# Kernel tuning notes

Hardware: AMD Instinct MI355X
Metric: run time of the kernel (lower is better)

## Reference

```python
import jax, jax.numpy as jnp
import numpy as np

FEA_DIM = 256
NUM_HEADS = 8
B, N = 32, 48


def setup_inputs() -> dict:
    key = jax.random.key(0)
    ks = jax.random.split(key, 30)
    d = FEA_DIM
    inp = {
        "async_fea": jax.random.normal(ks[0], (B, N, d), dtype=jnp.float32),
        "sync_fea": jax.random.normal(ks[1], (B, N, d), dtype=jnp.float32),
        "async_adj": jax.random.randint(ks[2], (B, N, N), 0, 2, dtype=jnp.int32),
        "sync_adj": jax.random.randint(ks[3], (B, N, N), 0, 2, dtype=jnp.int32),
    }
    i = 4
    for pref in ("a_", "s_"):
        for nm in ("Wq", "Wk", "Wv", "Wo", "Wm"):
            inp[pref + nm] = 0.02 * jax.random.normal(ks[i], (d, d), dtype=jnp.float32); i += 1
            inp[pref + nm.replace("W", "b")] = 0.02 * jax.random.normal(ks[i], (d,), dtype=jnp.float32); i += 1
    return inp


def _aggregate(x_src, adj, fallback, Wq, bq, Wk, bk, Wv, bv, Wo, bo, Wm, bm):
    """For each target t: self-attention among neighbor set {s : adj[b,s,t] > 0}
    of x_src, mean-pool over neighbors, divide by count again, linear map.
    Targets with no neighbors fall back to `fallback`."""
    Bb, Nn, D = x_src.shape
    H = NUM_HEADS
    dh = D // H
    q = (x_src @ Wq.T + bq).reshape(Bb, Nn, H, dh)
    k = (x_src @ Wk.T + bk).reshape(Bb, Nn, H, dh)
    v = (x_src @ Wv.T + bv).reshape(Bb, Nn, H, dh)
    # shared pairwise scores among source nodes: [B, H, Q, K]
    scores = jnp.einsum("bqhd,bkhd->bhqk", q, k) / jnp.sqrt(jnp.float32(dh))
    # neighbor mask per target: adj[b, s, t] > 0 -> m[b, t, s]
    m = jnp.transpose(adj > 0, (0, 2, 1))  # [B, T, S] bool
    # per-target masked softmax over keys: logits [B, T, H, Q, K]
    key_bias = jnp.where(m[:, :, None, None, :], 0.0, -1e9)
    attn = jax.nn.softmax(scores[:, None] + key_bias, axis=-1)  # [B,T,H,Q,K]
    out = jnp.einsum("bthqk,bkhd->bthqd", attn, v).reshape(Bb, Nn, Nn, D)  # [B,T,Q,D]
    out = out @ Wo.T + bo
    mf = m.astype(out.dtype)  # [B, T, Q]
    cnt = mf.sum(-1)  # [B, T]
    denom = jnp.maximum(cnt, 1.0)
    # torch: mean over valid queries, then / edge_cnt  => sum / cnt^2
    pooled = jnp.einsum("btq,btqd->btd", mf, out) / (denom * denom)[..., None]
    mapped = pooled @ Wm.T + bm
    return jnp.where((cnt > 0)[..., None], mapped, fallback)


def reference(async_fea, sync_fea, async_adj, sync_adj,
              a_Wq, a_bq, a_Wk, a_bk, a_Wv, a_bv, a_Wo, a_bo, a_Wm, a_bm,
              s_Wq, s_bq, s_Wk, s_bk, s_Wv, s_bv, s_Wo, s_bo, s_Wm, s_bm):
    refined_async = _aggregate(sync_fea, sync_adj, async_fea,
                               a_Wq, a_bq, a_Wk, a_bk, a_Wv, a_bv, a_Wo, a_bo, a_Wm, a_bm)
    refined_sync = _aggregate(async_fea, async_adj, sync_fea,
                              s_Wq, s_bq, s_Wk, s_bk, s_Wv, s_bv, s_Wo, s_bo, s_Wm, s_bm)
    return jnp.concatenate([refined_async, refined_sync, async_fea, sync_fea], axis=2)
```

## Files before the change

### kernel.cpp

```cpp
#include <hip/hip_runtime.h>

#define DD 256
#define HH 8
#define NN 48
#define BB 32

typedef __attribute__((ext_vector_type(8))) short short8v;
typedef __attribute__((ext_vector_type(4))) float f32x4;

__device__ __forceinline__ unsigned short f2bf(float f) {
    union { float f; unsigned u; } v; v.f = f;
    unsigned u = v.u;
    return (unsigned short)((u + 0x7FFFu + ((u >> 16) & 1u)) >> 16);
}

__device__ __forceinline__ short8v cvt8(const float* p) {
    float4 lo = *(const float4*)p;
    float4 hi = *(const float4*)(p + 4);
    union { uint4 u; short8v s; } r;
    asm("v_cvt_pk_bf16_f32 %0, %1, %2" : "=v"(r.u.x) : "v"(lo.x), "v"(lo.y));
    asm("v_cvt_pk_bf16_f32 %0, %1, %2" : "=v"(r.u.y) : "v"(lo.z), "v"(lo.w));
    asm("v_cvt_pk_bf16_f32 %0, %1, %2" : "=v"(r.u.z) : "v"(hi.x), "v"(hi.y));
    asm("v_cvt_pk_bf16_f32 %0, %1, %2" : "=v"(r.u.w) : "v"(hi.z), "v"(hi.w));
    return r.s;
}

__global__ __launch_bounds__(256) void qkv_fold(
    const float* __restrict__ async_fea, const float* __restrict__ sync_fea,
    const float* __restrict__ aWq, const float* __restrict__ abq,
    const float* __restrict__ aWk, const float* __restrict__ abk,
    const float* __restrict__ aWv, const float* __restrict__ abv,
    const float* __restrict__ aWm, const float* __restrict__ aWo, const float* __restrict__ abo,
    const float* __restrict__ sWq, const float* __restrict__ sbq,
    const float* __restrict__ sWk, const float* __restrict__ sbk,
    const float* __restrict__ sWv, const float* __restrict__ sbv,
    const float* __restrict__ sWm, const float* __restrict__ sWo, const float* __restrict__ sbo,
    float* __restrict__ QKV0, float* __restrict__ QKV1,
    unsigned short* __restrict__ Wcb0, unsigned short* __restrict__ Wcb1,
    float* __restrict__ bc0, float* __restrict__ bc1)
{
    __shared__ float smem[2304];
    int bid = blockIdx.x, tid = threadIdx.x;
    int wave = tid >> 6, lane = tid & 63;
    int l15 = lane & 15, l16 = (lane >> 4) << 3;

    if (bid < 576) {
        int agg = bid / 288, rem = bid % 288;
        int rt = rem / 12, ct = rem % 12;
        int row0 = rt * 64 + wave * 16;
        int col0 = ct * 64;
        int mat = ct >> 2;
        const float* X = agg ? async_fea : sync_fea;
        const float* W;
        const float* bias;
        if (agg == 0) {
            W    = (mat == 0) ? aWq : (mat == 1) ? aWk : aWv;
            bias = (mat == 0) ? abq : (mat == 1) ? abk : abv;
        } else {
            W    = (mat == 0) ? sWq : (mat == 1) ? sWk : sWv;
            bias = (mat == 0) ? sbq : (mat == 1) ? sbk : sbv;
        }
        const float* Xp = X + (row0 + l15) * 256 + l16;
        const float* Wp = W + ((ct & 3) * 64 + l15) * 256 + l16;
        f32x4 acc[4] = {{0,0,0,0},{0,0,0,0},{0,0,0,0},{0,0,0,0}};
        #pragma unroll
        for (int kk = 0; kk < 256; kk += 32) {
            short8v a = cvt8(Xp + kk);
            #pragma unroll
            for (int j = 0; j < 4; ++j) {
                short8v b = cvt8(Wp + j * 16 * 256 + kk);
                acc[j] = __builtin_amdgcn_mfma_f32_16x16x32_bf16(a, b, acc[j], 0, 0, 0);
            }
        }
        float* outQ = agg ? QKV1 : QKV0;
        #pragma unroll
        for (int j = 0; j < 4; ++j) {
            float bv = bias[(ct & 3) * 64 + j * 16 + l15];
            #pragma unroll
            for (int i = 0; i < 4; ++i) {
                int m = ((lane >> 4) << 2) + i;
                outQ[(row0 + m) * 768 + col0 + j * 16 + l15] = acc[j][i] + bv;
            }
        }
    } else {
        int fid = bid - 576;
        int agg = fid >> 4, tile = fid & 15;
        int cb = (tile >> 2) * 64, db = (tile & 3) * 64;
        const float* Wm = agg ? sWm : aWm;
        const float* Wo = agg ? sWo : aWo;
        const float* bo = agg ? sbo : abo;
        unsigned short* Wcb = agg ? Wcb1 : Wcb0;
        float* bc = agg ? bc1 : bc0;
        int crow = cb + wave * 16 + l15;
        const float* Wmp = Wm + crow * 256 + l16;
        f32x4 acc[4] = {{0,0,0,0},{0,0,0,0},{0,0,0,0},{0,0,0,0}};
        for (int ch = 0; ch < 8; ++ch) {
            __syncthreads();
            #pragma unroll
            for (int l = 0; l < 8; ++l) {
                int e = l * 256 + tid;
                int ii = e >> 6, dd = e & 63;
                smem[dd * 36 + ii] = Wo[(ch * 32 + ii) * 256 + db + dd];
            }
            __syncthreads();
            short8v a = cvt8(Wmp + ch * 32);
            #pragma unroll
            for (int j = 0; j < 4; ++j) {
                float* sp = &smem[(j * 16 + l15) * 36 + l16];
                float4 lo = *(const float4*)sp;
                float4 hi = *(const float4*)(sp + 4);
                union { uint4 u; short8v s; } rb;
                asm("v_cvt_pk_bf16_f32 %0, %1, %2" : "=v"(rb.u.x) : "v"(lo.x), "v"(lo.y));
                asm("v_cvt_pk_bf16_f32 %0, %1, %2" : "=v"(rb.u.y) : "v"(lo.z), "v"(lo.w));
                asm("v_cvt_pk_bf16_f32 %0, %1, %2" : "=v"(rb.u.z) : "v"(hi.x), "v"(hi.y));
                asm("v_cvt_pk_bf16_f32 %0, %1, %2" : "=v"(rb.u.w) : "v"(hi.z), "v"(hi.w));
                acc[j] = __builtin_amdgcn_mfma_f32_16x16x32_bf16(a, rb.s, acc[j], 0, 0, 0);
            }
        }
        #pragma unroll
        for (int j = 0; j < 4; ++j)
            #pragma unroll
            for (int i = 0; i < 4; ++i) {
                int c = cb + wave * 16 + ((lane >> 4) << 2) + i;
                int d = db + j * 16 + l15;
                Wcb[c * 256 + d] = f2bf(acc[j][i]);
            }
        if ((tile & 3) == 0) {
            int r = tid >> 2, s = tid & 3;
            const float* wmr = Wm + (cb + r) * 256 + s * 64;
            const float* bor = bo + s * 64;
            float a = 0.f;
            #pragma unroll
            for (int i = 0; i < 64; ++i) a += wmr[i] * bor[i];
            a += __shfl_xor(a, 1);
            a += __shfl_xor(a, 2);
            if (s == 0) bc[cb + r] = a;
        }
    }
}

__global__ __launch_bounds__(384) void mega_kernel(
    const float* __restrict__ QKV0, const float* __restrict__ QKV1,
    const int* __restrict__ sync_adj, const int* __restrict__ async_adj,
    const unsigned short* __restrict__ Wcb0, const unsigned short* __restrict__ Wcb1,
    const float* __restrict__ bc0, const float* __restrict__ bc1,
    const float* __restrict__ abm, const float* __restrict__ sbm,
    const float* __restrict__ async_fea, const float* __restrict__ sync_fea,
    float* __restrict__ out)
{
    __shared__ float E_lds[8 * 48 * 49];
    __shared__ float msk[12 * 48];
    __shared__ float invd[12][384];
    __shared__ float yv[12][384];
    __shared__ unsigned short P_lds[16 * 264];
    __shared__ float cnt_l[12];

    int bid = blockIdx.x, tid = threadIdx.x;
    int agg = bid >> 7, rem = bid & 127;
    int b = rem >> 2, tg = rem & 3;
    int wave = tid >> 6, lane = tid & 63;
    int l15 = lane & 15, g = lane >> 4, l16 = g << 3;

    const float* QKV = agg ? QKV1 : QKV0;
    const int*   adj = agg ? async_adj : sync_adj;
    const float* fb  = agg ? sync_fea : async_fea;
    int row_base = b * 48 + tg * 12;

    {
        const float4* fb4 = (const float4*)fb;
        float4* out4 = (float4*)out;
        #pragma unroll
        for (int l = 0; l < 2; ++l) {
            int e = l * 384 + tid;
            int r = e >> 6, c = e & 63;
            out4[(row_base + r) * 256 + 128 + agg * 64 + c] =
                fb4[(row_base + r) * 64 + c];
        }
    }

    for (int e = tid; e < 576; e += 384) {
        int tt = e / 48, s = e % 48;
        msk[tt * 48 + s] = (adj[(b * 48 + s) * 48 + tg * 12 + tt] > 0) ? 1.f : 0.f;
    }

    const float scale = 0.17677669529663687f;
    #pragma unroll
    for (int jj = 0; jj < 4; ++jj) {
        int job = wave * 4 + jj;
        int h = job / 3, qt = job % 3;
        short8v a = cvt8(QKV + (b * 48 + qt * 16 + l15) * 768 + h * 32 + l16);
        f32x4 acc[3];
        #pragma unroll
        for (int kt = 0; kt < 3; ++kt) {
            short8v kb = cvt8(QKV + (b * 48 + kt * 16 + l15) * 768 + 256 + h * 32 + l16);
            f32x4 z = {0.f, 0.f, 0.f, 0.f};
            acc[kt] = __builtin_amdgcn_mfma_f32_16x16x32_bf16(a, kb, z, 0, 0, 0);
        }
        float sc[3][4], rm[4];
        #pragma unroll
        for (int i = 0; i < 4; ++i) {
            #pragma unroll
            for (int kt = 0; kt < 3; ++kt) sc[kt][i] = acc[kt][i] * scale;
            rm[i] = fmaxf(fmaxf(sc[0][i], sc[1][i]), sc[2][i]);
        }
        #pragma unroll
        for (int m = 1; m <= 8; m <<= 1) {
            #pragma unroll
            for (int i = 0; i < 4; ++i) rm[i] = fmaxf(rm[i], __shfl_xor(rm[i], m));
        }
        #pragma unroll
        for (int kt = 0; kt < 3; ++kt)
            #pragma unroll
            for (int i = 0; i < 4; ++i)
                E_lds[(h * 48 + qt * 16 + g * 4 + i) * 49 + kt * 16 + l15] =
                    __expf(sc[kt][i] - rm[i]);
    }
    __syncthreads();

    if (tid < 12) {
        float c = 0.f;
        for (int s = 0; s < 48; ++s) c += msk[tid * 48 + s];
        cnt_l[tid] = c;
    }

    {
        float erow[48];
        #pragma unroll
        for (int kk = 0; kk < 48; ++kk) erow[kk] = E_lds[tid * 49 + kk];
        int q = tid % 48;
        #pragma unroll
        for (int tt = 0; tt < 12; ++tt) {
            const float4* m4p = (const float4*)&msk[tt * 48];
            float s = 0.f;
            #pragma unroll
            for (int k4 = 0; k4 < 12; ++k4) {
                float4 m4 = m4p[k4];
                s += m4.x * erow[4 * k4] + m4.y * erow[4 * k4 + 1]
                   + m4.z * erow[4 * k4 + 2] + m4.w * erow[4 * k4 + 3];
            }
            float mq = msk[tt * 48 + q];
            invd[tt][tid] = (mq > 0.f) ? (1.f / s) : 0.f;
        }
    }
    __syncthreads();

    {
        int h = tid / 48, k = tid % 48;
        float ecol[48];
        #pragma unroll
        for (int q = 0; q < 48; ++q) ecol[q] = E_lds[(h * 48 + q) * 49 + k];
        #pragma unroll
        for (int tt = 0; tt < 12; ++tt) {
            const float4* iv4 = (const float4*)&invd[tt][h * 48];
            float s = 0.f;
            #pragma unroll
            for (int q4 = 0; q4 < 12; ++q4) {
                float4 v = iv4[q4];
                s += v.x * ecol[4 * q4] + v.y * ecol[4 * q4 + 1]
                   + v.z * ecol[4 * q4 + 2] + v.w * ecol[4 * q4 + 3];
            }
            yv[tt][tid] = msk[tt * 48 + k] * s;
        }
    }
    __syncthreads();

    {
        for (int e = tid; e < 768; e += 384) {
            int tt = e >> 6, d4 = e & 63;
            int h = d4 >> 3;
            const float* yr = &yv[tt][h * 48];
            const float* Vp = QKV + b * 48 * 768 + 512 + d4 * 4;
            float4 p = {0.f, 0.f, 0.f, 0.f};
            for (int k = 0; k < 48; ++k) {
                float yval = yr[k];
                float4 vv = *(const float4*)(Vp + k * 768);
                p.x += yval * vv.x; p.y += yval * vv.y;
                p.z += yval * vv.z; p.w += yval * vv.w;
            }
            unsigned r0, r1;
            asm("v_cvt_pk_bf16_f32 %0, %1, %2" : "=v"(r0) : "v"(p.x), "v"(p.y));
            asm("v_cvt_pk_bf16_f32 %0, %1, %2" : "=v"(r1) : "v"(p.z), "v"(p.w));
            uint2 pk; pk.x = r0; pk.y = r1;
            *(uint2*)&P_lds[tt * 264 + d4 * 4] = pk;
        }
    }
    __syncthreads();

    const unsigned short* Wcb = agg ? Wcb1 : Wcb0;
    const float* bc = agg ? bc1 : bc0;
    const float* bm = agg ? sbm : abm;
    for (int ct = wave; ct < 16; ct += 6) {
        f32x4 acc = {0.f, 0.f, 0.f, 0.f};
        const unsigned short* Wp = Wcb + (ct * 16 + l15) * 256 + l16;
        const unsigned short* Pp = &P_lds[l15 * 264 + l16];
        #pragma unroll
        for (int kk = 0; kk < 8; ++kk) {
            short8v a = *(const short8v*)(Pp + kk * 32);
            short8v bfr = *(const short8v*)(Wp + kk * 32);
            acc = __builtin_amdgcn_mfma_f32_16x16x32_bf16(a, bfr, acc, 0, 0, 0);
        }
        int c = ct * 16 + l15;
        float bcv = bc[c], bmv = bm[c];
        #pragma unroll
        for (int i = 0; i < 4; ++i) {
            int t = g * 4 + i;
            if (t < 12) {
                int grow = row_base + t;
                float cn = cnt_l[t];
                float val;
                if (cn > 0.f) {
                    float inv1 = 1.f / cn;
                    val = acc[i] * inv1 * inv1 + bcv * inv1 + bmv;
                } else {
                    val = fb[grow * 256 + c];
                }
                out[grow * 1024 + agg * 256 + c] = val;
            }
        }
    }
}

extern "C" void kernel_launch(void* const* d_in, const int* in_sizes, int n_in,
                              void* d_out, int out_size, void* d_ws, size_t ws_size,
                              hipStream_t stream)
{
    const float* async_fea = (const float*)d_in[0];
    const float* sync_fea  = (const float*)d_in[1];
    const int*   async_adj = (const int*)d_in[2];
    const int*   sync_adj  = (const int*)d_in[3];
    const float* aWq = (const float*)d_in[4];
    const float* abq = (const float*)d_in[5];
    const float* aWk = (const float*)d_in[6];
    const float* abk = (const float*)d_in[7];
    const float* aWv = (const float*)d_in[8];
    const float* abv = (const float*)d_in[9];
    const float* aWo = (const float*)d_in[10];
    const float* abo = (const float*)d_in[11];
    const float* aWm = (const float*)d_in[12];
    const float* abm = (const float*)d_in[13];
    const float* sWq = (const float*)d_in[14];
    const float* sbq = (const float*)d_in[15];
    const float* sWk = (const float*)d_in[16];
    const float* sbk = (const float*)d_in[17];
    const float* sWv = (const float*)d_in[18];
    const float* sbv = (const float*)d_in[19];
    const float* sWo = (const float*)d_in[20];
    const float* sbo = (const float*)d_in[21];
    const float* sWm = (const float*)d_in[22];
    const float* sbm = (const float*)d_in[23];

    float* ws_f = (float*)d_ws;
    float* QKV0 = ws_f;
    float* QKV1 = QKV0 + 1179648;
    float* bc0  = QKV1 + 1179648;
    float* bc1  = bc0 + 256;
    unsigned short* Wcb0 = (unsigned short*)(bc1 + 256);
    unsigned short* Wcb1 = Wcb0 + 65536;

    qkv_fold<<<608, 256, 0, stream>>>(
        async_fea, sync_fea,
        aWq, abq, aWk, abk, aWv, abv, aWm, aWo, abo,
        sWq, sbq, sWk, sbk, sWv, sbv, sWm, sWo, sbo,
        QKV0, QKV1, Wcb0, Wcb1, bc0, bc1);
    mega_kernel<<<256, 384, 0, stream>>>(
        QKV0, QKV1, sync_adj, async_adj, Wcb0, Wcb1, bc0, bc1,
        abm, sbm, async_fea, sync_fea, (float*)d_out);
}
```

Measured before the change: 61.36 us.

## Fuse projection and attention into one cooperative kernel with grid syncs and bf16 intermediates

Replaces the two-kernel pipeline with one cooperative launch of 256 blocks. Per-wave jobs compute the Q/K/V projections and the Wm·Wo fold, then the score/exp stage is spread across all waves, with grid-wide syncs between phases. Intermediates (Q, K, transposed V, exp scores) are stored in bf16 instead of fp32, and the V contraction now runs on MFMA instead of scalar loops. The aim is to cut a launch and its gap, raise parallelism in the score stage and halve intermediate traffic. The cost is two grid barriers, a global round trip for the exp scores, and extra bf16 rounding.

```diff
diff --git a/kernel.cpp b/kernel.cpp
--- a/kernel.cpp
+++ b/kernel.cpp
@@ -1,9 +1,7 @@
 #include <hip/hip_runtime.h>
-
-#define DD 256
-#define HH 8
-#define NN 48
-#define BB 32
+#include <hip/hip_cooperative_groups.h>
+
+namespace cg = cooperative_groups;
 
 typedef __attribute__((ext_vector_type(8))) short short8v;
 typedef __attribute__((ext_vector_type(4))) float f32x4;
@@ -13,7 +11,9 @@
     unsigned u = v.u;
     return (unsigned short)((u + 0x7FFFu + ((u >> 16) & 1u)) >> 16);
 }
-
+__device__ __forceinline__ float bf2f(unsigned short u) {
+    union { unsigned u; float f; } v; v.u = ((unsigned)u) << 16; return v.f;
+}
 __device__ __forceinline__ short8v cvt8(const float* p) {
     float4 lo = *(const float4*)p;
     float4 hi = *(const float4*)(p + 4);
@@ -24,178 +24,147 @@
     asm("v_cvt_pk_bf16_f32 %0, %1, %2" : "=v"(r.u.w) : "v"(hi.z), "v"(hi.w));
     return r.s;
 }
-
-__global__ __launch_bounds__(256) void qkv_fold(
-    const float* __restrict__ async_fea, const float* __restrict__ sync_fea,
-    const float* __restrict__ aWq, const float* __restrict__ abq,
-    const float* __restrict__ aWk, const float* __restrict__ abk,
-    const float* __restrict__ aWv, const float* __restrict__ abv,
-    const float* __restrict__ aWm, const float* __restrict__ aWo, const float* __restrict__ abo,
-    const float* __restrict__ sWq, const float* __restrict__ sbq,
-    const float* __restrict__ sWk, const float* __restrict__ sbk,
-    const float* __restrict__ sWv, const float* __restrict__ sbv,
-    const float* __restrict__ sWm, const float* __restrict__ sWo, const float* __restrict__ sbo,
-    float* __restrict__ QKV0, float* __restrict__ QKV1,
-    unsigned short* __restrict__ Wcb0, unsigned short* __restrict__ Wcb1,
-    float* __restrict__ bc0, float* __restrict__ bc1)
+__device__ __forceinline__ short8v ld8(const unsigned short* p) {
+    return *(const short8v*)p;
+}
+
+struct GigaParams {
+    const float *async_fea, *sync_fea;
+    const int *async_adj, *sync_adj;
+    const float *aWq, *abq, *aWk, *abk, *aWv, *abv, *aWo, *abo, *aWm, *abm;
+    const float *sWq, *sbq, *sWk, *sbk, *sWv, *sbv, *sWo, *sbo, *sWm, *sbm;
+    unsigned short *Qb, *Kb, *VT, *Wcb, *Eg;
+    float *bc;
+    float *out;
+};
+
+__global__ __launch_bounds__(384) void giga_kernel(GigaParams p)
 {
-    __shared__ float smem[2304];
-    int bid = blockIdx.x, tid = threadIdx.x;
-    int wave = tid >> 6, lane = tid & 63;
-    int l15 = lane & 15, l16 = (lane >> 4) << 3;
-
-    if (bid < 576) {
-        int agg = bid / 288, rem = bid % 288;
-        int rt = rem / 12, ct = rem % 12;
-        int row0 = rt * 64 + wave * 16;
-        int col0 = ct * 64;
-        int mat = ct >> 2;
-        const float* X = agg ? async_fea : sync_fea;
-        const float* W;
-        const float* bias;
-        if (agg == 0) {
-            W    = (mat == 0) ? aWq : (mat == 1) ? aWk : aWv;
-            bias = (mat == 0) ? abq : (mat == 1) ? abk : abv;
-        } else {
-            W    = (mat == 0) ? sWq : (mat == 1) ? sWk : sWv;
-            bias = (mat == 0) ? sbq : (mat == 1) ? sbk : sbv;
-        }
-        const float* Xp = X + (row0 + l15) * 256 + l16;
-        const float* Wp = W + ((ct & 3) * 64 + l15) * 256 + l16;
-        f32x4 acc[4] = {{0,0,0,0},{0,0,0,0},{0,0,0,0},{0,0,0,0}};
-        #pragma unroll
-        for (int kk = 0; kk < 256; kk += 32) {
-            short8v a = cvt8(Xp + kk);
-            #pragma unroll
-            for (int j = 0; j < 4; ++j) {
-                short8v b = cvt8(Wp + j * 16 * 256 + kk);
-                acc[j] = __builtin_amdgcn_mfma_f32_16x16x32_bf16(a, b, acc[j], 0, 0, 0);
-            }
-        }
-        float* outQ = agg ? QKV1 : QKV0;
-        #pragma unroll
-        for (int j = 0; j < 4; ++j) {
-            float bv = bias[(ct & 3) * 64 + j * 16 + l15];
-            #pragma unroll
-            for (int i = 0; i < 4; ++i) {
-                int m = ((lane >> 4) << 2) + i;
-                outQ[(row0 + m) * 768 + col0 + j * 16 + l15] = acc[j][i] + bv;
-            }
-        }
-    } else {
-        int fid = bid - 576;
-        int agg = fid >> 4, tile = fid & 15;
-        int cb = (tile >> 2) * 64, db = (tile & 3) * 64;
-        const float* Wm = agg ? sWm : aWm;
-        const float* Wo = agg ? sWo : aWo;
-        const float* bo = agg ? sbo : abo;
-        unsigned short* Wcb = agg ? Wcb1 : Wcb0;
-        float* bc = agg ? bc1 : bc0;
-        int crow = cb + wave * 16 + l15;
-        const float* Wmp = Wm + crow * 256 + l16;
-        f32x4 acc[4] = {{0,0,0,0},{0,0,0,0},{0,0,0,0},{0,0,0,0}};
-        for (int ch = 0; ch < 8; ++ch) {
-            __syncthreads();
-            #pragma unroll
-            for (int l = 0; l < 8; ++l) {
-                int e = l * 256 + tid;
-                int ii = e >> 6, dd = e & 63;
-                smem[dd * 36 + ii] = Wo[(ch * 32 + ii) * 256 + db + dd];
-            }
-            __syncthreads();
-            short8v a = cvt8(Wmp + ch * 32);
-            #pragma unroll
-            for (int j = 0; j < 4; ++j) {
-                float* sp = &smem[(j * 16 + l15) * 36 + l16];
-                float4 lo = *(const float4*)sp;
-                float4 hi = *(const float4*)(sp + 4);
-                union { uint4 u; short8v s; } rb;
-                asm("v_cvt_pk_bf16_f32 %0, %1, %2" : "=v"(rb.u.x) : "v"(lo.x), "v"(lo.y));
-                asm("v_cvt_pk_bf16_f32 %0, %1, %2" : "=v"(rb.u.y) : "v"(lo.z), "v"(lo.w));
-                asm("v_cvt_pk_bf16_f32 %0, %1, %2" : "=v"(rb.u.z) : "v"(hi.x), "v"(hi.y));
-                asm("v_cvt_pk_bf16_f32 %0, %1, %2" : "=v"(rb.u.w) : "v"(hi.z), "v"(hi.w));
-                acc[j] = __builtin_amdgcn_mfma_f32_16x16x32_bf16(a, rb.s, acc[j], 0, 0, 0);
-            }
-        }
-        #pragma unroll
-        for (int j = 0; j < 4; ++j)
-            #pragma unroll
-            for (int i = 0; i < 4; ++i) {
-                int c = cb + wave * 16 + ((lane >> 4) << 2) + i;
-                int d = db + j * 16 + l15;
-                Wcb[c * 256 + d] = f2bf(acc[j][i]);
-            }
-        if ((tile & 3) == 0) {
-            int r = tid >> 2, s = tid & 3;
-            const float* wmr = Wm + (cb + r) * 256 + s * 64;
-            const float* bor = bo + s * 64;
-            float a = 0.f;
-            #pragma unroll
-            for (int i = 0; i < 64; ++i) a += wmr[i] * bor[i];
-            a += __shfl_xor(a, 1);
-            a += __shfl_xor(a, 2);
-            if (s == 0) bc[cb + r] = a;
-        }
-    }
-}
-
-__global__ __launch_bounds__(384) void mega_kernel(
-    const float* __restrict__ QKV0, const float* __restrict__ QKV1,
-    const int* __restrict__ sync_adj, const int* __restrict__ async_adj,
-    const unsigned short* __restrict__ Wcb0, const unsigned short* __restrict__ Wcb1,
-    const float* __restrict__ bc0, const float* __restrict__ bc1,
-    const float* __restrict__ abm, const float* __restrict__ sbm,
-    const float* __restrict__ async_fea, const float* __restrict__ sync_fea,
-    float* __restrict__ out)
-{
-    __shared__ float E_lds[8 * 48 * 49];
+    __shared__ unsigned short E_l[8 * 48 * 50];
     __shared__ float msk[12 * 48];
-    __shared__ float invd[12][384];
-    __shared__ float yv[12][384];
+    __shared__ float invd[12 * 384];
+    __shared__ unsigned short yv_b[16 * 520];
     __shared__ unsigned short P_lds[16 * 264];
     __shared__ float cnt_l[12];
 
-    int bid = blockIdx.x, tid = threadIdx.x;
-    int agg = bid >> 7, rem = bid & 127;
-    int b = rem >> 2, tg = rem & 3;
-    int wave = tid >> 6, lane = tid & 63;
-    int l15 = lane & 15, g = lane >> 4, l16 = g << 3;
-
-    const float* QKV = agg ? QKV1 : QKV0;
-    const int*   adj = agg ? async_adj : sync_adj;
-    const float* fb  = agg ? sync_fea : async_fea;
-    int row_base = b * 48 + tg * 12;
+    const int bid = blockIdx.x, tid = threadIdx.x;
+    const int wave = tid >> 6, lane = tid & 63;
+    const int l15 = lane & 15, g = lane >> 4, l16 = g << 3;
+    const int w = bid * 6 + wave;
+
+    #pragma unroll
+    for (int rep = 0; rep < 2; ++rep) {
+        int job = w + rep * 1536;
+        if (job >= 2432) break;
+        if (job < 2304) {
+            int t = job / 768;
+            int r = job % 768;
+            int agg = r / 384, rr = r % 384;
+            int rowtile = rr >> 2, coltile = rr & 3;
+            int row0 = rowtile * 16, col0 = coltile * 64;
+            const float* X = agg ? p.async_fea : p.sync_fea;
+            const float* W; const float* bias;
+            if (agg == 0) {
+                W    = (t == 0) ? p.aWq : (t == 1) ? p.aWk : p.aWv;
+                bias = (t == 0) ? p.abq : (t == 1) ? p.abk : p.abv;
+            } else {
+                W    = (t == 0) ? p.sWq : (t == 1) ? p.sWk : p.sWv;
+                bias = (t == 0) ? p.sbq : (t == 1) ? p.sbk : p.sbv;
+            }
+            const float* Xp = X + (row0 + l15) * 256 + l16;
+            const float* Wp = W + (col0 + l15) * 256 + l16;
+            f32x4 acc[4] = {{0,0,0,0},{0,0,0,0},{0,0,0,0},{0,0,0,0}};
+            #pragma unroll
+            for (int kk = 0; kk < 8; ++kk) {
+                short8v a = cvt8(Xp + kk * 32);
+                #pragma unroll
+                for (int j = 0; j < 4; ++j) {
+                    short8v b = cvt8(Wp + j * 16 * 256 + kk * 32);
+                    acc[j] = __builtin_amdgcn_mfma_f32_16x16x32_bf16(a, b, acc[j], 0, 0, 0);
+                }
+            }
+            if (t < 2) {
+                unsigned short* dst = (t == 0 ? p.Qb : p.Kb) + agg * 393216;
+                #pragma unroll
+                for (int j = 0; j < 4; ++j) {
+                    int c = col0 + j * 16 + l15;
+                    float bv = bias[c];
+                    #pragma unroll
+                    for (int i = 0; i < 4; ++i) {
+                        int row = row0 + g * 4 + i;
+                        dst[row * 256 + c] = f2bf(acc[j][i] + bv);
+                    }
+                }
+            } else {
+                int bq = row0 / 48, nb = row0 % 48;
+                unsigned short* vt = p.VT + agg * 524288 + bq * 16384;
+                #pragma unroll
+                for (int j = 0; j < 4; ++j) {
+                    int d = col0 + j * 16 + l15;
+                    float bv = bias[d];
+                    #pragma unroll
+                    for (int i = 0; i < 4; ++i) {
+                        int m = g * 4 + i;
+                        vt[d * 64 + nb + m] = f2bf(acc[j][i] + bv);
+                        if (rowtile % 3 == 2) vt[d * 64 + 48 + m] = 0;
+                    }
+                }
+            }
+        } else {
+            int jid2 = job - 2304;
+            int agg = jid2 >> 6, r2 = jid2 & 63;
+            int ct16 = r2 >> 2, dt64 = r2 & 3;
+            const float* Wm = agg ? p.sWm : p.aWm;
+            const float* Wo = agg ? p.sWo : p.aWo;
+            const float* bo = agg ? p.sbo : p.abo;
+            const float* Wmp = Wm + (ct16 * 16 + l15) * 256 + l16;
+            f32x4 acc[4] = {{0,0,0,0},{0,0,0,0},{0,0,0,0},{0,0,0,0}};
+            for (int kk = 0; kk < 8; ++kk) {
+                short8v a = cvt8(Wmp + kk * 32);
+                #pragma unroll
+                for (int jf = 0; jf < 4; ++jf) {
+                    union { unsigned short u[8]; short8v s; } bf;
+                    #pragma unroll
+                    for (int jj = 0; jj < 8; ++jj)
+                        bf.u[jj] = f2bf(Wo[(kk * 32 + l16 + jj) * 256 + dt64 * 64 + jf * 16 + l15]);
+                    acc[jf] = __builtin_amdgcn_mfma_f32_16x16x32_bf16(a, bf.s, acc[jf], 0, 0, 0);
+                }
+            }
+            unsigned short* Wcb = p.Wcb + agg * 65536;
+            #pragma unroll
+            for (int jf = 0; jf < 4; ++jf)
+                #pragma unroll
+                for (int i = 0; i < 4; ++i)
+                    Wcb[(ct16 * 16 + g * 4 + i) * 256 + dt64 * 64 + jf * 16 + l15] = f2bf(acc[jf][i]);
+            if (dt64 == 0) {
+                const float* wmr = Wm + (ct16 * 16 + l15) * 256 + g * 64;
+                const float* bor = bo + g * 64;
+                float s = 0.f;
+                #pragma unroll
+                for (int i2 = 0; i2 < 64; ++i2) s += wmr[i2] * bor[i2];
+                s += __shfl_xor(s, 16);
+                s += __shfl_xor(s, 32);
+                if (g == 0) p.bc[agg * 256 + ct16 * 16 + l15] = s;
+            }
+        }
+    }
+
+    cg::this_grid().sync();
 
     {
-        const float4* fb4 = (const float4*)fb;
-        float4* out4 = (float4*)out;
-        #pragma unroll
-        for (int l = 0; l < 2; ++l) {
-            int e = l * 384 + tid;
-            int r = e >> 6, c = e & 63;
-            out4[(row_base + r) * 256 + 128 + agg * 64 + c] =
-                fb4[(row_base + r) * 64 + c];
-        }
-    }
-
-    for (int e = tid; e < 576; e += 384) {
-        int tt = e / 48, s = e % 48;
-        msk[tt * 48 + s] = (adj[(b * 48 + s) * 48 + tg * 12 + tt] > 0) ? 1.f : 0.f;
-    }
-
-    const float scale = 0.17677669529663687f;
-    #pragma unroll
-    for (int jj = 0; jj < 4; ++jj) {
-        int job = wave * 4 + jj;
-        int h = job / 3, qt = job % 3;
-        short8v a = cvt8(QKV + (b * 48 + qt * 16 + l15) * 768 + h * 32 + l16);
+        int agg = w / 768, r = w % 768;
+        int b = r / 24, j24 = r % 24, h = j24 / 3, qt = j24 % 3;
+        const unsigned short* Qbp = p.Qb + agg * 393216;
+        const unsigned short* Kbp = p.Kb + agg * 393216;
+        short8v a = ld8(Qbp + (b * 48 + qt * 16 + l15) * 256 + h * 32 + l16);
         f32x4 acc[3];
         #pragma unroll
         for (int kt = 0; kt < 3; ++kt) {
-            short8v kb = cvt8(QKV + (b * 48 + kt * 16 + l15) * 768 + 256 + h * 32 + l16);
+            short8v kb = ld8(Kbp + (b * 48 + kt * 16 + l15) * 256 + h * 32 + l16);
             f32x4 z = {0.f, 0.f, 0.f, 0.f};
             acc[kt] = __builtin_amdgcn_mfma_f32_16x16x32_bf16(a, kb, z, 0, 0, 0);
         }
+        const float scale = 0.17677669529663687f;
         float sc[3][4], rm[4];
         #pragma unroll
         for (int i = 0; i < 4; ++i) {
@@ -204,117 +173,157 @@
             rm[i] = fmaxf(fmaxf(sc[0][i], sc[1][i]), sc[2][i]);
         }
         #pragma unroll
-        for (int m = 1; m <= 8; m <<= 1) {
+        for (int m = 1; m <= 8; m <<= 1)
             #pragma unroll
             for (int i = 0; i < 4; ++i) rm[i] = fmaxf(rm[i], __shfl_xor(rm[i], m));
-        }
+        unsigned short* Egp = p.Eg + agg * 589824 + b * 18432 + h * 2304;
         #pragma unroll
         for (int kt = 0; kt < 3; ++kt)
             #pragma unroll
             for (int i = 0; i < 4; ++i)
-                E_lds[(h * 48 + qt * 16 + g * 4 + i) * 49 + kt * 16 + l15] =
-                    __expf(sc[kt][i] - rm[i]);
+                Egp[(qt * 16 + g * 4 + i) * 48 + kt * 16 + l15] =
+                    f2bf(__expf(sc[kt][i] - rm[i]));
     }
-    __syncthreads();
-
-    if (tid < 12) {
-        float c = 0.f;
-        for (int s = 0; s < 48; ++s) c += msk[tid * 48 + s];
-        cnt_l[tid] = c;
-    }
+
+    cg::this_grid().sync();
 
     {
+        int agg = bid >> 7, rem = bid & 127, b2 = rem >> 2, tg = rem & 3;
+        int row_base = b2 * 48 + tg * 12;
+        const float* fb = agg ? p.sync_fea : p.async_fea;
+        const int* adj = agg ? p.async_adj : p.sync_adj;
+
+        {
+            const float4* fb4 = (const float4*)fb;
+            float4* out4 = (float4*)p.out;
+            #pragma unroll
+            for (int l = 0; l < 2; ++l) {
+                int e = l * 384 + tid;
+                int r = e >> 6, c = e & 63;
+                out4[(row_base + r) * 256 + 128 + agg * 64 + c] =
+                    fb4[(row_base + r) * 64 + c];
+            }
+        }
+
         float erow[48];
-        #pragma unroll
-        for (int kk = 0; kk < 48; ++kk) erow[kk] = E_lds[tid * 49 + kk];
-        int q = tid % 48;
-        #pragma unroll
-        for (int tt = 0; tt < 12; ++tt) {
-            const float4* m4p = (const float4*)&msk[tt * 48];
-            float s = 0.f;
-            #pragma unroll
-            for (int k4 = 0; k4 < 12; ++k4) {
-                float4 m4 = m4p[k4];
-                s += m4.x * erow[4 * k4] + m4.y * erow[4 * k4 + 1]
-                   + m4.z * erow[4 * k4 + 2] + m4.w * erow[4 * k4 + 3];
-            }
-            float mq = msk[tt * 48 + q];
-            invd[tt][tid] = (mq > 0.f) ? (1.f / s) : 0.f;
-        }
-    }
-    __syncthreads();
-
-    {
-        int h = tid / 48, k = tid % 48;
-        float ecol[48];
-        #pragma unroll
-        for (int q = 0; q < 48; ++q) ecol[q] = E_lds[(h * 48 + q) * 49 + k];
-        #pragma unroll
-        for (int tt = 0; tt < 12; ++tt) {
-            const float4* iv4 = (const float4*)&invd[tt][h * 48];
-            float s = 0.f;
-            #pragma unroll
-            for (int q4 = 0; q4 < 12; ++q4) {
-                float4 v = iv4[q4];
-                s += v.x * ecol[4 * q4] + v.y * ecol[4 * q4 + 1]
-                   + v.z * ecol[4 * q4 + 2] + v.w * ecol[4 * q4 + 3];
-            }
-            yv[tt][tid] = msk[tt * 48 + k] * s;
-        }
-    }
-    __syncthreads();
-
-    {
-        for (int e = tid; e < 768; e += 384) {
-            int tt = e >> 6, d4 = e & 63;
-            int h = d4 >> 3;
-            const float* yr = &yv[tt][h * 48];
-            const float* Vp = QKV + b * 48 * 768 + 512 + d4 * 4;
-            float4 p = {0.f, 0.f, 0.f, 0.f};
-            for (int k = 0; k < 48; ++k) {
-                float yval = yr[k];
-                float4 vv = *(const float4*)(Vp + k * 768);
-                p.x += yval * vv.x; p.y += yval * vv.y;
-                p.z += yval * vv.z; p.w += yval * vv.w;
-            }
-            unsigned r0, r1;
-            asm("v_cvt_pk_bf16_f32 %0, %1, %2" : "=v"(r0) : "v"(p.x), "v"(p.y));
-            asm("v_cvt_pk_bf16_f32 %0, %1, %2" : "=v"(r1) : "v"(p.z), "v"(p.w));
-            uint2 pk; pk.x = r0; pk.y = r1;
-            *(uint2*)&P_lds[tt * 264 + d4 * 4] = pk;
-        }
-    }
-    __syncthreads();
-
-    const unsigned short* Wcb = agg ? Wcb1 : Wcb0;
-    const float* bc = agg ? bc1 : bc0;
-    const float* bm = agg ? sbm : abm;
-    for (int ct = wave; ct < 16; ct += 6) {
-        f32x4 acc = {0.f, 0.f, 0.f, 0.f};
-        const unsigned short* Wp = Wcb + (ct * 16 + l15) * 256 + l16;
-        const unsigned short* Pp = &P_lds[l15 * 264 + l16];
-        #pragma unroll
-        for (int kk = 0; kk < 8; ++kk) {
-            short8v a = *(const short8v*)(Pp + kk * 32);
-            short8v bfr = *(const short8v*)(Wp + kk * 32);
-            acc = __builtin_amdgcn_mfma_f32_16x16x32_bf16(a, bfr, acc, 0, 0, 0);
-        }
-        int c = ct * 16 + l15;
-        float bcv = bc[c], bmv = bm[c];
-        #pragma unroll
-        for (int i = 0; i < 4; ++i) {
-            int t = g * 4 + i;
-            if (t < 12) {
-                int grow = row_base + t;
-                float cn = cnt_l[t];
-                float val;
-                if (cn > 0.f) {
-                    float inv1 = 1.f / cn;
-                    val = acc[i] * inv1 * inv1 + bcv * inv1 + bmv;
-                } else {
-                    val = fb[grow * 256 + c];
-                }
-                out[grow * 1024 + agg * 256 + c] = val;
+        {
+            const uint4* src = (const uint4*)(p.Eg + agg * 589824 + b2 * 18432 + tid * 48);
+            uint* El_u = (uint*)E_l;
+            #pragma unroll
+            for (int v = 0; v < 6; ++v) {
+                uint4 u4 = src[v];
+                unsigned uu[4] = {u4.x, u4.y, u4.z, u4.w};
+                #pragma unroll
+                for (int c = 0; c < 4; ++c) {
+                    El_u[tid * 25 + v * 4 + c] = uu[c];
+                    union { unsigned u; float f; } lo, hi;
+                    lo.u = uu[c] << 16;
+                    hi.u = uu[c] & 0xFFFF0000u;
+                    erow[v * 8 + c * 2]     = lo.f;
+                    erow[v * 8 + c * 2 + 1] = hi.f;
+                }
+            }
+        }
+        for (int e = tid; e < 576; e += 384) {
+            int tt = e / 48, s = e % 48;
+            msk[tt * 48 + s] = (adj[(b2 * 48 + s) * 48 + tg * 12 + tt] > 0) ? 1.f : 0.f;
+        }
+        {
+            uint* yz = (uint*)yv_b;
+            for (int e = tid; e < 4160; e += 384) yz[e] = 0u;
+        }
+        __syncthreads();
+        if (tid < 12) {
+            float c = 0.f;
+            for (int s = 0; s < 48; ++s) c += msk[tid * 48 + s];
+            cnt_l[tid] = c;
+        }
+
+        {
+            int q = tid % 48;
+            #pragma unroll
+            for (int tt = 0; tt < 12; ++tt) {
+                const float4* m4p = (const float4*)&msk[tt * 48];
+                float ss = 0.f;
+                #pragma unroll
+                for (int k4 = 0; k4 < 12; ++k4) {
+                    float4 m4 = m4p[k4];
+                    ss += m4.x * erow[4 * k4] + m4.y * erow[4 * k4 + 1]
+                        + m4.z * erow[4 * k4 + 2] + m4.w * erow[4 * k4 + 3];
+                }
+                invd[tt * 384 + tid] = (msk[tt * 48 + q] > 0.f) ? (1.f / ss) : 0.f;
+            }
+        }
+        __syncthreads();
+
+        {
+            int h2 = tid / 48, k = tid % 48;
+            float ecol[48];
+            #pragma unroll
+            for (int q = 0; q < 48; ++q) ecol[q] = bf2f(E_l[(h2 * 48 + q) * 50 + k]);
+            #pragma unroll
+            for (int tt = 0; tt < 12; ++tt) {
+                const float4* iv4 = (const float4*)&invd[tt * 384 + h2 * 48];
+                float ss = 0.f;
+                #pragma unroll
+                for (int q4 = 0; q4 < 12; ++q4) {
+                    float4 v = iv4[q4];
+                    ss += v.x * ecol[4 * q4] + v.y * ecol[4 * q4 + 1]
+                        + v.z * ecol[4 * q4 + 2] + v.w * ecol[4 * q4 + 3];
+                }
+                yv_b[tt * 520 + h2 * 64 + k] = f2bf(msk[tt * 48 + k] * ss);
+            }
+        }
+        __syncthreads();
+
+        for (int dt = wave; dt < 16; dt += 6) {
+            int h = dt >> 1;
+            int d = dt * 16 + l15;
+            const unsigned short* yb = yv_b + l15 * 520 + h * 64;
+            short8v a0 = ld8(yb + l16);
+            short8v a1 = ld8(yb + 32 + l16);
+            const unsigned short* vtp = p.VT + agg * 524288 + (b2 * 256 + d) * 64;
+            short8v b0 = ld8(vtp + l16);
+            short8v b1 = ld8(vtp + 32 + l16);
+            f32x4 acc = {0.f, 0.f, 0.f, 0.f};
+            acc = __builtin_amdgcn_mfma_f32_16x16x32_bf16(a0, b0, acc, 0, 0, 0);
+            acc = __builtin_amdgcn_mfma_f32_16x16x32_bf16(a1, b1, acc, 0, 0, 0);
+            #pragma unroll
+            for (int i = 0; i < 4; ++i)
+                P_lds[(g * 4 + i) * 264 + dt * 16 + l15] = f2bf(acc[i]);
+        }
+        __syncthreads();
+
+        const unsigned short* Wcb = p.Wcb + agg * 65536;
+        const float* bc = p.bc + agg * 256;
+        const float* bm = agg ? p.sbm : p.abm;
+        for (int ct = wave; ct < 16; ct += 6) {
+            f32x4 acc = {0.f, 0.f, 0.f, 0.f};
+            const unsigned short* Wp = Wcb + (ct * 16 + l15) * 256 + l16;
+            const unsigned short* Pp = P_lds + l15 * 264 + l16;
+            #pragma unroll
+            for (int kk = 0; kk < 8; ++kk) {
+                short8v a = ld8(Pp + kk * 32);
+                short8v bfr = ld8(Wp + kk * 32);
+                acc = __builtin_amdgcn_mfma_f32_16x16x32_bf16(a, bfr, acc, 0, 0, 0);
+            }
+            int c = ct * 16 + l15;
+            float bcv = bc[c], bmv = bm[c];
+            #pragma unroll
+            for (int i = 0; i < 4; ++i) {
+                int t = g * 4 + i;
+                if (t < 12) {
+                    int grow = row_base + t;
+                    float cn = cnt_l[t];
+                    float val;
+                    if (cn > 0.f) {
+                        float inv1 = 1.f / cn;
+                        val = acc[i] * inv1 * inv1 + bcv * inv1 + bmv;
+                    } else {
+                        val = fb[grow * 256 + c];
+                    }
+                    p.out[grow * 1024 + agg * 256 + c] = val;
+                }
             }
         }
     }
@@ -324,45 +333,32 @@
                               void* d_out, int out_size, void* d_ws, size_t ws_size,
                               hipStream_t stream)
 {
-    const float* async_fea = (const float*)d_in[0];
-    const float* sync_fea  = (const float*)d_in[1];
-    const int*   async_adj = (const int*)d_in[2];
-    const int*   sync_adj  = (const int*)d_in[3];
-    const float* aWq = (const float*)d_in[4];
-    const float* abq = (const float*)d_in[5];
-    const float* aWk = (const float*)d_in[6];
-    const float* abk = (const float*)d_in[7];
-    const float* aWv = (const float*)d_in[8];
-    const float* abv = (const float*)d_in[9];
-    const float* aWo = (const float*)d_in[10];
-    const float* abo = (const float*)d_in[11];
-    const float* aWm = (const float*)d_in[12];
-    const float* abm = (const float*)d_in[13];
-    const float* sWq = (const float*)d_in[14];
-    const float* sbq = (const float*)d_in[15];
-    const float* sWk = (const float*)d_in[16];
-    const float* sbk = (const float*)d_in[17];
-    const float* sWv = (const float*)d_in[18];
-    const float* sbv = (const float*)d_in[19];
-    const float* sWo = (const float*)d_in[20];
-    const float* sbo = (const float*)d_in[21];
-    const float* sWm = (const float*)d_in[22];
-    const float* sbm = (const float*)d_in[23];
-
-    float* ws_f = (float*)d_ws;
-    float* QKV0 = ws_f;
-    float* QKV1 = QKV0 + 1179648;
-    float* bc0  = QKV1 + 1179648;
-    float* bc1  = bc0 + 256;
-    unsigned short* Wcb0 = (unsigned short*)(bc1 + 256);
-    unsigned short* Wcb1 = Wcb0 + 65536;
-
-    qkv_fold<<<608, 256, 0, stream>>>(
-        async_fea, sync_fea,
-        aWq, abq, aWk, abk, aWv, abv, aWm, aWo, abo,
-        sWq, sbq, sWk, sbk, sWv, sbv, sWm, sWo, sbo,
-        QKV0, QKV1, Wcb0, Wcb1, bc0, bc1);
-    mega_kernel<<<256, 384, 0, stream>>>(
-        QKV0, QKV1, sync_adj, async_adj, Wcb0, Wcb1, bc0, bc1,
-        abm, sbm, async_fea, sync_fea, (float*)d_out);
-}
+    GigaParams p;
+    p.async_fea = (const float*)d_in[0];
+    p.sync_fea  = (const float*)d_in[1];
+    p.async_adj = (const int*)d_in[2];
+    p.sync_adj  = (const int*)d_in[3];
+    p.aWq = (const float*)d_in[4];   p.abq = (const float*)d_in[5];
+    p.aWk = (const float*)d_in[6];   p.abk = (const float*)d_in[7];
+    p.aWv = (const float*)d_in[8];   p.abv = (const float*)d_in[9];
+    p.aWo = (const float*)d_in[10];  p.abo = (const float*)d_in[11];
+    p.aWm = (const float*)d_in[12];  p.abm = (const float*)d_in[13];
+    p.sWq = (const float*)d_in[14];  p.sbq = (const float*)d_in[15];
+    p.sWk = (const float*)d_in[16];  p.sbk = (const float*)d_in[17];
+    p.sWv = (const float*)d_in[18];  p.sbv = (const float*)d_in[19];
+    p.sWo = (const float*)d_in[20];  p.sbo = (const float*)d_in[21];
+    p.sWm = (const float*)d_in[22];  p.sbm = (const float*)d_in[23];
+
+    unsigned short* us = (unsigned short*)d_ws;
+    p.Qb  = us;
+    p.Kb  = p.Qb + 786432;
+    p.VT  = p.Kb + 786432;
+    p.Wcb = p.VT + 1048576;
+    p.Eg  = p.Wcb + 131072;
+    p.bc  = (float*)(p.Eg + 1179648);
+    p.out = (float*)d_out;
+
+    void* args[] = { &p };
+    hipLaunchCooperativeKernel((void*)giga_kernel, dim3(256), dim3(384),
+                               args, 0, stream);
+}
```

After: 132.5 us. 116% more time.
